# Optimization experiments

Measured on AMD Instinct MI355X. Metric: run time of the kernel, lower is better.

Reference implementation:

```python
import jax, jax.numpy as jnp
import numpy as np

M, K, N = 8192, 4096, 4096
INT8_MAX = 127.0


def setup_inputs() -> dict:
    key = jax.random.key(0)
    k1, k2, k3, k4 = jax.random.split(key, 4)
    inp = jax.random.normal(k1, (M, K), dtype=jnp.float32)
    # int8 weight [out_features, in_features]
    weight = jax.random.randint(k2, (N, K), -128, 128, dtype=jnp.int32).astype(jnp.int8)
    # per-output-channel dequant scale
    weight_scale = jax.random.uniform(k3, (N,), dtype=jnp.float32, minval=1e-3, maxval=1e-2)
    bias = jax.random.normal(k4, (N,), dtype=jnp.float32) * 0.01
    return {"input": inp, "weight": weight, "weight_scale": weight_scale, "bias": bias}


def reference(input, weight, weight_scale, bias):
    # Dynamic per-token symmetric int8 quantization (scaled_int8_quant with
    # scale=None, azp=None, symmetric=True): scale_a = max|x| / 127 per row.
    absmax = jnp.max(jnp.abs(input), axis=-1, keepdims=True)  # [M, 1]
    scale_a = jnp.where(absmax > 0, absmax / INT8_MAX, jnp.float32(1.0))
    q = jnp.clip(jnp.round(input / scale_a), -128, 127).astype(jnp.int8)  # [M, K]
    # and per-column (weight_scale) dequant, plus bias, in input dtype.
    acc = jnp.matmul(q.astype(jnp.int32), weight.T.astype(jnp.int32))  # [M, N] int32
    out = acc.astype(jnp.float32) * scale_a * weight_scale[None, :] + bias[None, :]
    return out.astype(input.dtype)
```

## Files before the change

### kernel.cpp

```cpp
#include <hip/hip_runtime.h>
#include <cstdint>

typedef __attribute__((ext_vector_type(4))) int int32x4;

#define GLOBAL_AS __attribute__((address_space(1)))
#define LDS_AS    __attribute__((address_space(3)))

__global__ __launch_bounds__(256) void pack_w(
    const int* __restrict__ w32, uint32_t* __restrict__ w8_as_u32)
{
    const size_t i = (size_t)blockIdx.x * 256 + threadIdx.x;
    const int4 v = ((const int4*)w32)[i];
    w8_as_u32[i] = (v.x & 0xff) | ((v.y & 0xff) << 8) |
                   ((v.z & 0xff) << 16) | ((uint32_t)(v.w & 0xff) << 24);
}

__global__ __launch_bounds__(256) void quant_rows(
    const float* __restrict__ in, int8_t* __restrict__ q,
    float* __restrict__ sa, int K)
{
    const int row = blockIdx.x;
    const float4* rp = (const float4*)(in + (size_t)row * K);
    const int t = threadIdx.x;

    float amax = 0.f;
    float4 v[4];
#pragma unroll
    for (int i = 0; i < 4; ++i) {
        v[i] = rp[t + (i << 8)];
        amax = fmaxf(amax,
               fmaxf(fmaxf(fabsf(v[i].x), fabsf(v[i].y)),
                     fmaxf(fabsf(v[i].z), fabsf(v[i].w))));
    }

#pragma unroll
    for (int off = 32; off; off >>= 1)
        amax = fmaxf(amax, __shfl_xor(amax, off));
    __shared__ float smax[4];
    if ((t & 63) == 0) smax[t >> 6] = amax;
    __syncthreads();
    amax = fmaxf(fmaxf(smax[0], smax[1]), fmaxf(smax[2], smax[3]));

    const float scale = (amax > 0.f) ? (amax / 127.f) : 1.f;
    if (t == 0) sa[row] = scale;
    const float rs = 1.f / scale;

    int* qrow = (int*)(q + (size_t)row * K);
#pragma unroll
    for (int i = 0; i < 4; ++i) {
        int a = __float2int_rn(v[i].x * rs);
        int b = __float2int_rn(v[i].y * rs);
        int c = __float2int_rn(v[i].z * rs);
        int d = __float2int_rn(v[i].w * rs);
        a = max(-128, min(127, a));
        b = max(-128, min(127, b));
        c = max(-128, min(127, c));
        d = max(-128, min(127, d));
        qrow[t + (i << 8)] = (a & 0xff) | ((b & 0xff) << 8) |
                             ((c & 0xff) << 16) | ((d & 0xff) << 24);
    }
}

__device__ __forceinline__ void async_load16(const int8_t* g, int8_t* lds) {
    __builtin_amdgcn_global_load_lds((const GLOBAL_AS char*)g,
                                     (LDS_AS char*)lds, 16, 0, 0);
}

__global__ __launch_bounds__(512, 2) void w8a8_gemm(
    const int8_t* __restrict__ Aq, const int8_t* __restrict__ W,
    const float* __restrict__ sa, const float* __restrict__ wsc,
    const float* __restrict__ bias, float* __restrict__ out,
    int M, int N, int K)
{
    __shared__ int8_t lds[4 * 32768];

    const int NB = N >> 8;
    const int nwg = gridDim.x;
    const int cpx = nwg >> 3;
    const int wg = (blockIdx.x & 7) * cpx + (blockIdx.x >> 3);
    const int bm = wg / NB, bn = wg % NB;

    const int t = threadIdx.x;
    const int lane = t & 63, wid = t >> 6;
    const int wr = wid >> 2, wc = wid & 3;
    const int r = lane & 15, q4 = lane >> 4;

    const int srow = t >> 2;
    const int scol = (((t & 3) ^ ((t >> 3) & 3)) << 4);
    const int8_t* gA = Aq + ((size_t)bm * 256 + srow) * (size_t)K + scol;
    const int8_t* gB = W  + ((size_t)bn * 256 + srow) * (size_t)K + scol;
    const size_t half_stride = (size_t)128 * K;
    int8_t* ldsw = &lds[t * 16];

    auto stage = [&](int ring, int kbyte, int c) {
        const int8_t* src = (c < 2 ? gA : gB) + (size_t)(c & 1) * half_stride + kbyte;
        async_load16(src, ldsw + ring * 32768 + (c >> 1) * 16384 + (c & 1) * 8192);
    };

    const int xr = (r >> 1) & 3;
    const int ca = (q4 ^ xr) << 4;
    const int aoff0 = (wr * 128 + r) * 64 + ca;
    const int boff0 = 16384 + (wc * 64 + r) * 64 + ca;

    int32x4 acc[8][4];
#pragma unroll
    for (int m = 0; m < 8; ++m)
#pragma unroll
        for (int n = 0; n < 4; ++n)
            acc[m][n] = (int32x4){0, 0, 0, 0};

    const int NT = K >> 6;

#pragma unroll
    for (int c = 0; c < 4; ++c) stage(0, 0, c);
#pragma unroll
    for (int c = 0; c < 4; ++c) stage(1, 64, c);
    asm volatile("s_waitcnt vmcnt(4)" ::: "memory");
    asm volatile("s_barrier" ::: "memory");

    for (int g = 0; g < NT; ++g) {
        const int rbase = (g & 3) * 32768;
        const int sring = (g + 2) & 3;
        const int skb = (g + 2) << 6;
        const bool do_stage = (g + 2) < NT;
#pragma unroll
        for (int q = 0; q < 4; ++q) {
            const int qm = (q >> 1) * 4;
            const int qn = (q & 1) * 2;

            int32x4 af[4], bf[2];
#pragma unroll
            for (int i = 0; i < 4; ++i)
                af[i] = *(const int32x4*)&lds[rbase + aoff0 + (qm + i) * 1024];
#pragma unroll
            for (int j = 0; j < 2; ++j)
                bf[j] = *(const int32x4*)&lds[rbase + boff0 + (qn + j) * 1024];

            if (do_stage) stage(sring, skb, q);

            asm volatile("s_barrier" ::: "memory");
            __builtin_amdgcn_s_setprio(1);
#pragma unroll
            for (int i = 0; i < 4; ++i)
#pragma unroll
                for (int j = 0; j < 2; ++j)
                    acc[qm + i][qn + j] = __builtin_amdgcn_mfma_i32_16x16x64_i8(
                        af[i], bf[j], acc[qm + i][qn + j], 0, 0, 0);
            __builtin_amdgcn_s_setprio(0);

            if (q == 3) {
                if (g < NT - 2)
                    asm volatile("s_waitcnt vmcnt(4)" ::: "memory");
                else
                    asm volatile("s_waitcnt vmcnt(0)" ::: "memory");
            }
            asm volatile("s_barrier" ::: "memory");
        }
    }

    const int row0 = bm * 256 + wr * 128 + (q4 << 2);
    const int col0 = bn * 256 + wc * 64 + r;

    float sarow[8][4];
#pragma unroll
    for (int m = 0; m < 8; ++m)
#pragma unroll
        for (int j = 0; j < 4; ++j)
            sarow[m][j] = sa[row0 + (m << 4) + j];

#pragma unroll
    for (int n = 0; n < 4; ++n) {
        const int col = col0 + (n << 4);
        const float wn = wsc[col];
        const float bn_ = bias[col];
#pragma unroll
        for (int m = 0; m < 8; ++m) {
            const int rowb = row0 + (m << 4);
#pragma unroll
            for (int j = 0; j < 4; ++j) {
                out[(size_t)(rowb + j) * N + col] =
                    (float)acc[m][n][j] * sarow[m][j] * wn + bn_;
            }
        }
    }
}

extern "C" void kernel_launch(void* const* d_in, const int* in_sizes, int n_in,
                              void* d_out, int out_size, void* d_ws, size_t ws_size,
                              hipStream_t stream) {
    const float* inp  = (const float*)d_in[0];
    const int*   w32  = (const int*)d_in[1];
    const float* wsc  = (const float*)d_in[2];
    const float* bias = (const float*)d_in[3];
    float* out = (float*)d_out;

    const int N = in_sizes[2];
    const int K = in_sizes[1] / N;
    const int M = in_sizes[0] / K;

    int8_t* q  = (int8_t*)d_ws;
    float*  sa = (float*)((char*)d_ws + (size_t)M * K);
    int8_t* w8 = (int8_t*)((char*)d_ws + (size_t)M * K + (size_t)M * 4 + 256);

    const size_t nw4 = ((size_t)N * K) / 4;
    pack_w<<<(int)(nw4 / 256), 256, 0, stream>>>(w32, (uint32_t*)w8);

    quant_rows<<<M, 256, 0, stream>>>(inp, q, sa, K);

    const int nwg = (M / 256) * (N / 256);
    w8a8_gemm<<<nwg, 512, 0, stream>>>(q, w8, sa, wsc, bias, out, M, N, K);
}
```

Before: 211.1 us.

## Switch int8 GEMM from 16x16x64 to 32x32x32 MFMA tiles

Replaces the 16x16x64 int8 MFMA with the 32x32x32 variant, so each wave covers its 128x64 output tile with a 4x2 grid of 32x32 accumulators. The K-loop now runs two K sub-steps per 64-byte tile instead of four quadrant passes. LDS fragment addressing, the staging cadence (two stage calls per sub-step) and the epilogue row/column mapping are rewritten to match the 32x32 output layout. The aim is fewer LDS fragment reads per MFMA and larger MFMA ops, at the cost of halving the number of barrier-separated phases per tile, which may reduce load/compute overlap.

```diff
diff --git a/kernel.cpp b/kernel.cpp
--- a/kernel.cpp
+++ b/kernel.cpp
@@ -2,6 +2,7 @@
 #include <cstdint>
 
 typedef __attribute__((ext_vector_type(4))) int int32x4;
+typedef __attribute__((ext_vector_type(16))) int int32x16;
 
 #define GLOBAL_AS __attribute__((address_space(1)))
 #define LDS_AS    __attribute__((address_space(3)))
@@ -83,7 +84,8 @@
     const int t = threadIdx.x;
     const int lane = t & 63, wid = t >> 6;
     const int wr = wid >> 2, wc = wid & 3;
-    const int r = lane & 15, q4 = lane >> 4;
+    const int l31 = lane & 31, h = lane >> 5;
+    const int xr = (lane >> 1) & 3;
 
     const int srow = t >> 2;
     const int scol = (((t & 3) ^ ((t >> 3) & 3)) << 4);
@@ -97,17 +99,19 @@
         async_load16(src, ldsw + ring * 32768 + (c >> 1) * 16384 + (c & 1) * 8192);
     };
 
-    const int xr = (r >> 1) & 3;
-    const int ca = (q4 ^ xr) << 4;
-    const int aoff0 = (wr * 128 + r) * 64 + ca;
-    const int boff0 = 16384 + (wc * 64 + r) * 64 + ca;
-
-    int32x4 acc[8][4];
-#pragma unroll
-    for (int m = 0; m < 8; ++m)
-#pragma unroll
-        for (int n = 0; n < 4; ++n)
-            acc[m][n] = (int32x4){0, 0, 0, 0};
+    const int arow = (wr * 128 + l31) * 64;
+    const int brow = 16384 + (wc * 64 + l31) * 64;
+    const int cs0 = ((0 + h) ^ xr) << 4;
+    const int cs1 = ((2 + h) ^ xr) << 4;
+
+    int32x16 acc[4][2];
+#pragma unroll
+    for (int m = 0; m < 4; ++m)
+#pragma unroll
+        for (int n = 0; n < 2; ++n)
+#pragma unroll
+            for (int rgi = 0; rgi < 16; ++rgi)
+                acc[m][n][rgi] = 0;
 
     const int NT = K >> 6;
 
@@ -124,31 +128,33 @@
         const int skb = (g + 2) << 6;
         const bool do_stage = (g + 2) < NT;
 #pragma unroll
-        for (int q = 0; q < 4; ++q) {
-            const int qm = (q >> 1) * 4;
-            const int qn = (q & 1) * 2;
+        for (int kk = 0; kk < 2; ++kk) {
+            const int cs = kk ? cs1 : cs0;
 
             int32x4 af[4], bf[2];
 #pragma unroll
-            for (int i = 0; i < 4; ++i)
-                af[i] = *(const int32x4*)&lds[rbase + aoff0 + (qm + i) * 1024];
-#pragma unroll
-            for (int j = 0; j < 2; ++j)
-                bf[j] = *(const int32x4*)&lds[rbase + boff0 + (qn + j) * 1024];
-
-            if (do_stage) stage(sring, skb, q);
+            for (int m = 0; m < 4; ++m)
+                af[m] = *(const int32x4*)&lds[rbase + arow + m * 2048 + cs];
+#pragma unroll
+            for (int n = 0; n < 2; ++n)
+                bf[n] = *(const int32x4*)&lds[rbase + brow + n * 2048 + cs];
+
+            if (do_stage) {
+                stage(sring, skb, 2 * kk);
+                stage(sring, skb, 2 * kk + 1);
+            }
 
             asm volatile("s_barrier" ::: "memory");
             __builtin_amdgcn_s_setprio(1);
 #pragma unroll
-            for (int i = 0; i < 4; ++i)
-#pragma unroll
-                for (int j = 0; j < 2; ++j)
-                    acc[qm + i][qn + j] = __builtin_amdgcn_mfma_i32_16x16x64_i8(
-                        af[i], bf[j], acc[qm + i][qn + j], 0, 0, 0);
+            for (int m = 0; m < 4; ++m)
+#pragma unroll
+                for (int n = 0; n < 2; ++n)
+                    acc[m][n] = __builtin_amdgcn_mfma_i32_32x32x32_i8(
+                        af[m], bf[n], acc[m][n], 0, 0, 0);
             __builtin_amdgcn_s_setprio(0);
 
-            if (q == 3) {
+            if (kk == 1) {
                 if (g < NT - 2)
                     asm volatile("s_waitcnt vmcnt(4)" ::: "memory");
                 else
@@ -158,28 +164,25 @@
         }
     }
 
-    const int row0 = bm * 256 + wr * 128 + (q4 << 2);
-    const int col0 = bn * 256 + wc * 64 + r;
-
-    float sarow[8][4];
-#pragma unroll
-    for (int m = 0; m < 8; ++m)
-#pragma unroll
-        for (int j = 0; j < 4; ++j)
-            sarow[m][j] = sa[row0 + (m << 4) + j];
-
-#pragma unroll
-    for (int n = 0; n < 4; ++n) {
-        const int col = col0 + (n << 4);
-        const float wn = wsc[col];
-        const float bn_ = bias[col];
-#pragma unroll
-        for (int m = 0; m < 8; ++m) {
-            const int rowb = row0 + (m << 4);
-#pragma unroll
-            for (int j = 0; j < 4; ++j) {
-                out[(size_t)(rowb + j) * N + col] =
-                    (float)acc[m][n][j] * sarow[m][j] * wn + bn_;
+    const int col0 = bn * 256 + wc * 64 + l31;
+    const int row00 = bm * 256 + wr * 128 + 4 * h;
+
+#pragma unroll
+    for (int m = 0; m < 4; ++m) {
+        float sv[16];
+#pragma unroll
+        for (int rgi = 0; rgi < 16; ++rgi)
+            sv[rgi] = sa[row00 + m * 32 + (rgi & 3) + 8 * (rgi >> 2)];
+#pragma unroll
+        for (int n = 0; n < 2; ++n) {
+            const int col = col0 + n * 32;
+            const float wn = wsc[col];
+            const float bb = bias[col];
+#pragma unroll
+            for (int rgi = 0; rgi < 16; ++rgi) {
+                const int row = row00 + m * 32 + (rgi & 3) + 8 * (rgi >> 2);
+                out[(size_t)row * N + col] =
+                    (float)acc[m][n][rgi] * sv[rgi] * wn + bb;
             }
         }
     }
```

Result: faster. 200.2 us (-5.2%).
